# Kernel tuning notes

Measured on AMD Instinct MI355X. Metric: run time of the kernel, lower is better.

Reference implementation:

```python
import jax, jax.numpy as jnp
import numpy as np

BEAM = 8
MAX_LEN = 64
SOS_ID = 1
EOS_ID = 2
NEG = -1e30


def setup_inputs() -> dict:
    key = jax.random.key(0)
    ks = jax.random.split(key, 12)
    B, L, H, V, E = 16, 64, 1024, 32000, 1024
    s = 0.02
    return {
        "dec_hidden": jax.random.normal(ks[0], (B, H), jnp.float32),
        "q_enc_outputs": jax.random.normal(ks[1], (B, L, H), jnp.float32),
        "q_inputs_length": jax.random.randint(ks[2], (B,), 1, L + 1),
        "embedding": jax.random.normal(ks[3], (V, E), jnp.float32) * s,
        "W_ih": jax.random.normal(ks[4], (E, 3 * H), jnp.float32) * s,
        "W_hh": jax.random.normal(ks[5], (H, 3 * H), jnp.float32) * s,
        "b_ih": jnp.zeros((3 * H,), jnp.float32),
        "b_hh": jnp.zeros((3 * H,), jnp.float32),
        "W_c": jax.random.normal(ks[6], (2 * H, H), jnp.float32) * s,
        "W_out": jax.random.normal(ks[7], (H, V), jnp.float32) * s,
        "b_out": jnp.zeros((V,), jnp.float32),
    }


def _beam_search(dec_hidden, q_enc_outputs, q_inputs_length, embedding,
                 W_ih, W_hh, b_ih, b_hh, W_c, W_out, b_out):
    B, H = dec_hidden.shape
    L = q_enc_outputs.shape[1]
    V = W_out.shape[1]
    K = BEAM
    N = B * K
    pos_index = jnp.arange(B)[:, None] * K  # [B,1] offset of each batch's beam block

    # inflate encoder state beam_size times (beam is the inner dim: index = b*K + k)
    hidden = jnp.repeat(dec_hidden, K, axis=0)            # [N,H]
    q_enc = jnp.repeat(q_enc_outputs, K, axis=0)          # [N,L,H]
    q_len = jnp.repeat(q_inputs_length, K, axis=0)        # [N]
    len_mask = jnp.arange(L)[None, :] < q_len[:, None]    # [N,L]

    # only beam 0 of each batch starts live (score 0), rest -inf
    seq_scores = jnp.full((N,), NEG, jnp.float32).at[::K].set(0.0)
    dec_input = jnp.full((N,), SOS_ID, jnp.int32)

    def gru_cell(x, h):
        gx = x @ W_ih + b_ih
        gh = h @ W_hh + b_hh
        xr, xz, xn = jnp.split(gx, 3, axis=-1)
        hr, hz, hn = jnp.split(gh, 3, axis=-1)
        r = jax.nn.sigmoid(xr + hr)
        z = jax.nn.sigmoid(xz + hz)
        n = jnp.tanh(xn + r * hn)
        return (1.0 - z) * n + z * h

    def step(carry, _):
        hidden, seq_scores, dec_input = carry
        x = embedding[dec_input]                               # [N,E]
        h = gru_cell(x, hidden)                                # [N,H]
        # dot-product attention over encoder outputs
        att = jnp.einsum('nh,nlh->nl', h, q_enc) / jnp.sqrt(jnp.float32(H))
        att = jnp.where(len_mask, att, NEG)
        a = jax.nn.softmax(att, axis=-1)
        ctx = jnp.einsum('nl,nlh->nh', a, q_enc)
        o = jnp.tanh(jnp.concatenate([h, ctx], axis=-1) @ W_c)
        logits = o @ W_out + b_out                             # [N,V]
        logp = jax.nn.log_softmax(logits, axis=-1)
        # accumulate scores, flatten beams*vocab per batch, take top-K
        cand = (seq_scores[:, None] + logp).reshape(B, K * V)
        scores, idx = jax.lax.top_k(cand, K)                   # [B,K]
        symbols = (idx % V).reshape(N)
        preds = (idx // V + pos_index).reshape(N)              # predecessor beam rows
        new_hidden = h[preds]
        new_scores = scores.reshape(N)
        stored = new_scores                                     # stored before EOS mask
        new_scores = jnp.where(symbols == EOS_ID, NEG, new_scores)
        return (new_hidden, new_scores, symbols), (stored, preds, symbols)

    _, (all_scores, all_preds, all_syms) = jax.lax.scan(
        step, (hidden, seq_scores, dec_input), None, length=MAX_LEN)

    # backtrack: pick top-K final beams and trace predecessors backwards
    final_scores = all_scores[-1].reshape(B, K)
    sorted_score, sorted_idx = jax.lax.top_k(final_scores, K)
    t_pred = (sorted_idx + pos_index).reshape(N)

    def back(carry, xs):
        syms_t, preds_t = xs
        cur = syms_t[carry]
        return preds_t[carry], cur

    _, seq_rev = jax.lax.scan(back, t_pred, (all_syms[::-1], all_preds[::-1]))
    sequences = seq_rev[::-1].T.reshape(B, BEAM, MAX_LEN)
    return sorted_score, sequences


def reference(dec_hidden, q_enc_outputs, q_inputs_length, embedding,
              W_ih, W_hh, b_ih, b_hh, W_c, W_out, b_out):
    return _beam_search(dec_hidden, q_enc_outputs, q_inputs_length, embedding,
                        W_ih, W_hh, b_ih, b_hh, W_c, W_out, b_out)
```

## Files before the change

### kernel.cpp

```cpp
#include <hip/hip_runtime.h>
#include <cstdint>
#include <cstddef>
#include <climits>

#define Hdim 1024
#define Vdim 32000
#define Lq 64
#define Nrows 128
#define TMAX 64
#define NEGF (-1e30f)

__device__ __forceinline__ bool betterf(float av, int ai, float bv, int bi) {
  return (av > bv) || (av == bv && ai < bi);
}

__device__ __forceinline__ float tanh_xla(float x) {
  float ax = fabsf(x);
  float xc = fminf(fmaxf(x, -7.90531110763549805f), 7.90531110763549805f);
  float x2 = __fmul_rn(xc, xc);
  float p = -2.76076847742355e-16f;
  p = fmaf(p, x2, 2.00018790482477e-13f);
  p = fmaf(p, x2, -8.60467152213735e-11f);
  p = fmaf(p, x2, 5.12229709037114e-08f);
  p = fmaf(p, x2, 1.48572235717979e-05f);
  p = fmaf(p, x2, 6.37261928875436e-04f);
  p = fmaf(p, x2, 4.89352455891786e-03f);
  p = __fmul_rn(xc, p);
  float q = 1.19825839466702e-06f;
  q = fmaf(q, x2, 1.18534705686654e-04f);
  q = fmaf(q, x2, 2.26843463243900e-03f);
  q = fmaf(q, x2, 4.89352518554385e-03f);
  float r = __fdiv_rn(p, q);
  return (ax < 0.0004f) ? x : r;
}

__device__ __forceinline__ float sigmoid_xla(float x) {
  return __fadd_rn(0.5f, __fmul_rn(0.5f, tanh_xla(__fmul_rn(0.5f, x))));
}

__device__ __forceinline__ float exp_xla(float x) {
  x = fminf(x, 88.3762626647950f);
  x = fmaxf(x, -88.3762626647949f);
  float m = floorf(fmaf(x, 1.44269504088896341f, 0.5f));
  float r = fmaf(m, -0.693359375f, x);
  r = fmaf(m, 2.12194440e-4f, r);
  float r2 = __fmul_rn(r, r);
  float p = 1.9875691500e-4f;
  p = fmaf(p, r, 1.3981999507e-3f);
  p = fmaf(p, r, 8.3334519073e-3f);
  p = fmaf(p, r, 4.1665795894e-2f);
  p = fmaf(p, r, 1.6666665459e-1f);
  p = fmaf(p, r, 5.0000001201e-1f);
  p = fmaf(p, r2, r);
  p = __fadd_rn(p, 1.0f);
  int n = (int)m;
  float two_n = __int_as_float((n + 127) << 23);
  return __fmul_rn(p, two_n);
}

__device__ __forceinline__ float log_xla(float x) {
  int ix = __float_as_int(x);
  int e = ((ix >> 23) & 0xFF) - 126;
  float m = __int_as_float((ix & 0x007FFFFF) | 0x3F000000);
  if (m < 0.707106781186547524f) { e -= 1; m = __fadd_rn(m, m); }
  m = __fsub_rn(m, 1.0f);
  float z = __fmul_rn(m, m);
  float p = 7.0376836292e-2f;
  p = fmaf(p, m, -1.1514610310e-1f);
  p = fmaf(p, m, 1.1676998740e-1f);
  p = fmaf(p, m, -1.2420140846e-1f);
  p = fmaf(p, m, 1.4249322787e-1f);
  p = fmaf(p, m, -1.6668057665e-1f);
  p = fmaf(p, m, 2.0000714765e-1f);
  p = fmaf(p, m, -2.4999993993e-1f);
  p = fmaf(p, m, 3.3333331174e-1f);
  float ef = (float)e;
  float y = __fmul_rn(m, __fmul_rn(z, p));
  y = fmaf(ef, -2.12194440e-4f, y);
  y = fmaf(z, -0.5f, y);
  float res = __fadd_rn(m, y);
  res = fmaf(ef, 0.693359375f, res);
  return res;
}

__device__ __forceinline__ int bswz(int col) {
  return col ^ (((col >> 5) & 3) << 2);
}

template <int MT, int NT>
__device__ __forceinline__ void gemm_body(
    const float* __restrict__ A, int lda, const int* __restrict__ rowmap,
    const float* __restrict__ B, int ldb, const float* __restrict__ bias,
    float* __restrict__ C, int ldc, int K, int act, int n0, int m0)
{
  constexpr int RM = MT / 16, RN = NT / 16;
  constexpr int PA = MT + 4, PB = NT + 4;
  __shared__ float As[32][PA];
  __shared__ float Bs[32][PB];
  __shared__ int rows[MT];
  const int t = threadIdx.x;
  if (t < MT) rows[t] = rowmap ? rowmap[m0 + t] : (m0 + t);
  __syncthreads();
  const int tm = t >> 4, tn = t & 15;
  float acc[RM][RN] = {};
  for (int kt = 0; kt < K; kt += 32) {
#pragma unroll
    for (int i = 0; i < MT / 32; ++i) {
      int idx = t + i * 256;
      int m = idx >> 3, k4 = idx & 7;
      float4 v = *reinterpret_cast<const float4*>(
          &A[(size_t)rows[m] * lda + (size_t)(kt + k4 * 4)]);
      As[k4 * 4 + 0][m] = v.x;
      As[k4 * 4 + 1][m] = v.y;
      As[k4 * 4 + 2][m] = v.z;
      As[k4 * 4 + 3][m] = v.w;
    }
#pragma unroll
    for (int i = 0; i < NT / 32; ++i) {
      int idx = t + i * 256;
      int kk = idx / (NT / 4), n4 = idx % (NT / 4);
      float4 v = *reinterpret_cast<const float4*>(
          &B[(size_t)(kt + kk) * ldb + (size_t)(n0 + n4 * 4)]);
      *reinterpret_cast<float4*>(&Bs[kk][bswz(n4 * 4)]) = v;
    }
    __syncthreads();
#pragma unroll
    for (int kk = 0; kk < 32; ++kk) {
      float a[RM], bb[RN];
      if constexpr (RM == 2) {
        float2 v = *reinterpret_cast<const float2*>(&As[kk][tm * 2]);
        a[0] = v.x; a[1] = v.y;
      } else {
#pragma unroll
        for (int c = 0; c < RM / 4; ++c) {
          float4 v = *reinterpret_cast<const float4*>(&As[kk][tm * RM + c * 4]);
          a[c * 4 + 0] = v.x; a[c * 4 + 1] = v.y;
          a[c * 4 + 2] = v.z; a[c * 4 + 3] = v.w;
        }
      }
      if constexpr (RN == 2) {
        float2 v = *reinterpret_cast<const float2*>(&Bs[kk][tn * 2]);
        bb[0] = v.x; bb[1] = v.y;
      } else {
#pragma unroll
        for (int c = 0; c < RN / 4; ++c) {
          float4 v = *reinterpret_cast<const float4*>(
              &Bs[kk][bswz(tn * RN + c * 4)]);
          bb[c * 4 + 0] = v.x; bb[c * 4 + 1] = v.y;
          bb[c * 4 + 2] = v.z; bb[c * 4 + 3] = v.w;
        }
      }
#pragma unroll
      for (int i = 0; i < RM; ++i)
#pragma unroll
        for (int j = 0; j < RN; ++j)
          acc[i][j] = fmaf(a[i], bb[j], acc[i][j]);
    }
    __syncthreads();
  }
#pragma unroll
  for (int i = 0; i < RM; ++i) {
    int m = m0 + tm * RM + i;
#pragma unroll
    for (int j = 0; j < RN; ++j) {
      int n = n0 + tn * RN + j;
      float v = acc[i][j];
      if (bias) v = __fadd_rn(v, bias[n]);
      if (act == 1) v = tanh_xla(v);
      C[(size_t)m * ldc + n] = v;
    }
  }
}

__global__ __launch_bounds__(128, 2) void sgemm_logits(
    const float* __restrict__ A, const float* __restrict__ B,
    const float* __restrict__ bias, float* __restrict__ C)
{
  constexpr int MT = 128, NT = 128, RM = 8, RN = 16;
  constexpr int PA = MT + 4, PB = NT + 4;
  __shared__ float As[32][PA];
  __shared__ float Bs[32][PB];
  const int t = threadIdx.x;
  const int n0 = blockIdx.x * NT;
  const int tm = t >> 3, tn = t & 7;
  float acc[RM][RN] = {};
  for (int kt = 0; kt < 1024; kt += 32) {
#pragma unroll
    for (int i = 0; i < 8; ++i) {
      int idx = t + i * 128;
      int m = idx >> 3, k4 = idx & 7;
      float4 v = *reinterpret_cast<const float4*>(
          &A[(size_t)m * 1024 + (size_t)(kt + k4 * 4)]);
      As[k4 * 4 + 0][m] = v.x;
      As[k4 * 4 + 1][m] = v.y;
      As[k4 * 4 + 2][m] = v.z;
      As[k4 * 4 + 3][m] = v.w;
    }
#pragma unroll
    for (int i = 0; i < 8; ++i) {
      int idx = t + i * 128;
      int kk = idx >> 5, n4 = idx & 31;
      float4 v = *reinterpret_cast<const float4*>(
          &B[(size_t)(kt + kk) * 32000 + (size_t)(n0 + n4 * 4)]);
      *reinterpret_cast<float4*>(&Bs[kk][bswz(n4 * 4)]) = v;
    }
    __syncthreads();
#pragma unroll
    for (int kk = 0; kk < 32; ++kk) {
      float a[RM], bb[RN];
#pragma unroll
      for (int c = 0; c < 2; ++c) {
        float4 v = *reinterpret_cast<const float4*>(&As[kk][tm * RM + c * 4]);
        a[c * 4 + 0] = v.x; a[c * 4 + 1] = v.y;
        a[c * 4 + 2] = v.z; a[c * 4 + 3] = v.w;
      }
#pragma unroll
      for (int c = 0; c < 4; ++c) {
        float4 v = *reinterpret_cast<const float4*>(
            &Bs[kk][bswz(tn * RN + c * 4)]);
        bb[c * 4 + 0] = v.x; bb[c * 4 + 1] = v.y;
        bb[c * 4 + 2] = v.z; bb[c * 4 + 3] = v.w;
      }
#pragma unroll
      for (int i = 0; i < RM; ++i)
#pragma unroll
        for (int j = 0; j < RN; ++j)
          acc[i][j] = fmaf(a[i], bb[j], acc[i][j]);
    }
    __syncthreads();
  }
#pragma unroll
  for (int i = 0; i < RM; ++i) {
    int m = tm * RM + i;
#pragma unroll
    for (int j = 0; j < RN; ++j) {
      int n = n0 + tn * RN + j;
      float v = __fadd_rn(acc[i][j], bias[n]);
      C[(size_t)m * 32000 + n] = v;
    }
  }
}

__global__ __launch_bounds__(256) void gates_gemm(
    const float* __restrict__ emb, const int* __restrict__ symmap,
    const float* __restrict__ W_ih,
    const float* __restrict__ hprev, const int* __restrict__ hmap,
    const float* __restrict__ W_hh,
    float* __restrict__ gA, float* __restrict__ gB)
{
  if (blockIdx.z == 0)
    gemm_body<32, 64>(emb, 1024, symmap, W_ih, 3072, nullptr, gA, 3072, 1024, 0,
                      blockIdx.x * 64, blockIdx.y * 32);
  else
    gemm_body<32, 64>(hprev, 1024, hmap, W_hh, 3072, nullptr, gB, 3072, 1024, 0,
                      blockIdx.x * 64, blockIdx.y * 32);
}

__global__ __launch_bounds__(256) void sgemm_wc(
    const float* __restrict__ A2, const float* __restrict__ W_c,
    float* __restrict__ obuf)
{
  gemm_body<32, 32>(A2, 2048, nullptr, W_c, 1024, nullptr, obuf, 1024, 2048, 1,
                    blockIdx.x * 32, blockIdx.y * 32);
}

__global__ __launch_bounds__(256) void gru_attn(
    const float* __restrict__ gA, const float* __restrict__ gB,
    const float* __restrict__ b_ih, const float* __restrict__ b_hh,
    const float* __restrict__ hprev, const int* __restrict__ hmap,
    const float* __restrict__ q_enc, const int* __restrict__ q_len,
    float* __restrict__ hout, float* __restrict__ A2)
{
  int n = blockIdx.x;
  int b = n >> 3;
  int t = threadIdx.x;
  __shared__ float hsh[Hdim];
  __shared__ float att[Lq];
  __shared__ float ebuf[Lq];
  __shared__ float s_mx, s_sum;

  {
    int row = hmap[n];
    const float* hp = hprev + (size_t)row * Hdim;
    const float* a = gA + (size_t)n * 3 * Hdim;
    const float* g = gB + (size_t)n * 3 * Hdim;
    for (int j = t; j < Hdim; j += 256) {
      float xr = __fadd_rn(a[j],            b_ih[j]);
      float xz = __fadd_rn(a[Hdim + j],     b_ih[Hdim + j]);
      float xn = __fadd_rn(a[2 * Hdim + j], b_ih[2 * Hdim + j]);
      float hr = __fadd_rn(g[j],            b_hh[j]);
      float hz = __fadd_rn(g[Hdim + j],     b_hh[Hdim + j]);
      float hn = __fadd_rn(g[2 * Hdim + j], b_hh[2 * Hdim + j]);
      float r = sigmoid_xla(__fadd_rn(xr, hr));
      float z = sigmoid_xla(__fadd_rn(xz, hz));
      float t1 = __fmul_rn(r, hn);
      float nn = tanh_xla(__fadd_rn(xn, t1));
      float u1 = __fsub_rn(1.0f, z);
      float u2 = __fmul_rn(u1, nn);
      float u3 = __fmul_rn(z, hp[j]);
      float h = __fadd_rn(u2, u3);
      hout[(size_t)n * Hdim + j] = h;
      A2[(size_t)n * 2 * Hdim + j] = h;
      hsh[j] = h;
    }
  }
  __syncthreads();

  const float* q = q_enc + (size_t)b * Lq * Hdim;
  if (t < Lq) {
    const float4* h4 = reinterpret_cast<const float4*>(hsh);
    const float4* q4 = reinterpret_cast<const float4*>(q + (size_t)t * Hdim);
    float acc[8];
#pragma unroll
    for (int j = 0; j < 8; ++j) acc[j] = 0.f;
    for (int i = 0; i < 128; ++i) {
      float4 ha = h4[2 * i], hb = h4[2 * i + 1];
      float4 qa = q4[2 * i], qb = q4[2 * i + 1];
      acc[0] = fmaf(ha.x, qa.x, acc[0]);
      acc[1] = fmaf(ha.y, qa.y, acc[1]);
      acc[2] = fmaf(ha.z, qa.z, acc[2]);
      acc[3] = fmaf(ha.w, qa.w, acc[3]);
      acc[4] = fmaf(hb.x, qb.x, acc[4]);
      acc[5] = fmaf(hb.y, qb.y, acc[5]);
      acc[6] = fmaf(hb.z, qb.z, acc[6]);
      acc[7] = fmaf(hb.w, qb.w, acc[7]);
    }
    float b0 = __fadd_rn(acc[0], acc[4]);
    float b1 = __fadd_rn(acc[1], acc[5]);
    float b2 = __fadd_rn(acc[2], acc[6]);
    float b3 = __fadd_rn(acc[3], acc[7]);
    float c0 = __fadd_rn(b0, b2);
    float c1 = __fadd_rn(b1, b3);
    float dot = __fadd_rn(c0, c1);
    att[t] = __fdiv_rn(dot, 32.0f);
  }
  __syncthreads();
  if (t == 0) {
    int len = q_len[b];
    float mx = -INFINITY;
    for (int l = 0; l < Lq; ++l) {
      float v = (l < len) ? att[l] : NEGF;
      att[l] = v;
      mx = fmaxf(mx, v);
    }
    s_mx = mx;
  }
  __syncthreads();
  if (t < Lq) ebuf[t] = exp_xla(__fsub_rn(att[t], s_mx));
  __syncthreads();
  if (t == 0) {
    float acc[8];
#pragma unroll
    for (int j = 0; j < 8; ++j) acc[j] = 0.f;
    for (int i = 0; i < 8; ++i) {
#pragma unroll
      for (int j = 0; j < 8; ++j) acc[j] = __fadd_rn(acc[j], ebuf[i * 8 + j]);
    }
    float b0 = __fadd_rn(acc[0], acc[4]);
    float b1 = __fadd_rn(acc[1], acc[5]);
    float b2 = __fadd_rn(acc[2], acc[6]);
    float b3 = __fadd_rn(acc[3], acc[7]);
    float c0 = __fadd_rn(b0, b2);
    float c1 = __fadd_rn(b1, b3);
    s_sum = __fadd_rn(c0, c1);
  }
  __syncthreads();
  if (t < Lq) att[t] = __fdiv_rn(ebuf[t], s_sum);
  __syncthreads();
#pragma unroll
  for (int hh = 0; hh < 4; ++hh) {
    int h = t + hh * 256;
    float c = 0.f;
    for (int l = 0; l < Lq; ++l) c = fmaf(att[l], q[(size_t)l * Hdim + h], c);
    A2[(size_t)n * 2 * Hdim + Hdim + h] = c;
  }
}

__global__ __launch_bounds__(256) void lse_kernel(const float* __restrict__ logits,
                                                  float* __restrict__ ebuf,
                                                  float* __restrict__ mxA,
                                                  float* __restrict__ lseA)
{
  int n = blockIdx.x;
  const float* row = logits + (size_t)n * Vdim;
  float* erow = ebuf + (size_t)n * Vdim;
  int t = threadIdx.x;
  int lane = t & 63, w = t >> 6;
  const float4* row4 = reinterpret_cast<const float4*>(row);
  float4* erow4 = reinterpret_cast<float4*>(erow);
  float mx = -INFINITY;
  for (int i = t; i < 8000; i += 256) {
    float4 v = row4[i];
    mx = fmaxf(mx, fmaxf(fmaxf(v.x, v.y), fmaxf(v.z, v.w)));
  }
#pragma unroll
  for (int off = 32; off >= 1; off >>= 1) mx = fmaxf(mx, __shfl_xor(mx, off, 64));
  __shared__ float sm[4];
  __shared__ float lanes[8];
  if (lane == 0) sm[w] = mx;
  __syncthreads();
  mx = fmaxf(fmaxf(sm[0], sm[1]), fmaxf(sm[2], sm[3]));
  for (int i = t; i < 8000; i += 256) {
    float4 v = row4[i];
    float4 e;
    e.x = exp_xla(__fsub_rn(v.x, mx));
    e.y = exp_xla(__fsub_rn(v.y, mx));
    e.z = exp_xla(__fsub_rn(v.z, mx));
    e.w = exp_xla(__fsub_rn(v.w, mx));
    erow4[i] = e;
  }
  __syncthreads();
  if (t < 8) {
    float a = 0.f;
#pragma unroll 8
    for (int i = 0; i < 4000; ++i) a = __fadd_rn(a, erow[i * 8 + t]);
    lanes[t] = a;
  }
  __syncthreads();
  if (t == 0) {
    float b0 = __fadd_rn(lanes[0], lanes[4]);
    float b1 = __fadd_rn(lanes[1], lanes[5]);
    float b2 = __fadd_rn(lanes[2], lanes[6]);
    float b3 = __fadd_rn(lanes[3], lanes[7]);
    float c0 = __fadd_rn(b0, b2);
    float c1 = __fadd_rn(b1, b3);
    float s = __fadd_rn(c0, c1);
    mxA[n] = mx;
    lseA[n] = log_xla(s);
  }
}

__global__ __launch_bounds__(256) void topk_kernel(
    const float* __restrict__ logits, const float* __restrict__ mxA,
    const float* __restrict__ lseA, float* __restrict__ seq_scores,
    float* __restrict__ all_scores, int* __restrict__ all_preds,
    int* __restrict__ all_syms, int step)
{
  int b = blockIdx.x, t = threadIdx.x;
  __shared__ float s_seq[8], s_mx[8], s_lse[8];
  if (t < 8) {
    s_seq[t] = seq_scores[b * 8 + t];
    s_mx[t] = mxA[b * 8 + t];
    s_lse[t] = lseA[b * 8 + t];
  }
  __syncthreads();
  float lv[8]; int li[8];
#pragma unroll
  for (int r = 0; r < 8; ++r) { lv[r] = -INFINITY; li[r] = INT_MAX; }
  const float4* base4 = reinterpret_cast<const float4*>(logits + (size_t)b * 8 * Vdim);
  for (int c4 = t; c4 < 64000; c4 += 256) {
    float4 v4 = base4[c4];
    int cb = c4 * 4;
#pragma unroll
    for (int e = 0; e < 4; ++e) {
      int c = cb + e;
      int k = c / Vdim;
      float x = (e == 0) ? v4.x : (e == 1) ? v4.y : (e == 2) ? v4.z : v4.w;
      float sh = __fsub_rn(x, s_mx[k]);
      float lp = __fsub_rn(sh, s_lse[k]);
      float cand = __fadd_rn(s_seq[k], lp);
      if (betterf(cand, c, lv[7], li[7])) {
        lv[7] = cand; li[7] = c;
#pragma unroll
        for (int r = 7; r > 0; --r) {
          if (betterf(lv[r], li[r], lv[r - 1], li[r - 1])) {
            float tv = lv[r]; lv[r] = lv[r - 1]; lv[r - 1] = tv;
            int ti = li[r]; li[r] = li[r - 1]; li[r - 1] = ti;
          }
        }
      }
    }
  }
  __shared__ float sv[256][8];
  __shared__ int si[256][8];
#pragma unroll
  for (int r = 0; r < 8; ++r) { sv[t][r] = lv[r]; si[t][r] = li[r]; }
  __syncthreads();
  if (t == 0) {
    for (int u = 1; u < 256; ++u) {
#pragma unroll
      for (int r = 0; r < 8; ++r) {
        float v = sv[u][r]; int ix = si[u][r];
        if (betterf(v, ix, lv[7], li[7])) {
          lv[7] = v; li[7] = ix;
#pragma unroll
          for (int q = 7; q > 0; --q) {
            if (betterf(lv[q], li[q], lv[q - 1], li[q - 1])) {
              float tv = lv[q]; lv[q] = lv[q - 1]; lv[q - 1] = tv;
              int ti = li[q]; li[q] = li[q - 1]; li[q - 1] = ti;
            }
          }
        } else break;
      }
    }
#pragma unroll
    for (int r = 0; r < 8; ++r) {
      int idx = li[r];
      int sym = idx % Vdim;
      int pred = idx / Vdim + b * 8;
      int n = b * 8 + r;
      all_scores[step * Nrows + n] = lv[r];
      all_preds[step * Nrows + n] = pred;
      all_syms[step * Nrows + n] = sym;
      seq_scores[n] = (sym == 2) ? NEGF : lv[r];
    }
  }
}

__global__ void init_kernel(float* seq_scores, int* init_hmap, int* init_sym) {
  int t = threadIdx.x;
  if (t < 128) {
    seq_scores[t] = ((t & 7) == 0) ? 0.0f : NEGF;
    init_hmap[t] = t >> 3;
    init_sym[t] = 1;
  }
}

__global__ void final_topk(const float* __restrict__ all_scores,
                           int* __restrict__ tpred, float* __restrict__ out_scores) {
  int b = threadIdx.x;
  if (b >= 16) return;
  float v[8]; int ki[8];
#pragma unroll
  for (int k = 0; k < 8; ++k) { v[k] = all_scores[63 * Nrows + b * 8 + k]; ki[k] = k; }
#pragma unroll
  for (int p = 0; p < 7; ++p)
#pragma unroll
    for (int i = 0; i < 7; ++i) {
      if (!betterf(v[i], ki[i], v[i + 1], ki[i + 1])) {
        float tv = v[i]; v[i] = v[i + 1]; v[i + 1] = tv;
        int ti = ki[i]; ki[i] = ki[i + 1]; ki[i + 1] = ti;
      }
    }
#pragma unroll
  for (int j = 0; j < 8; ++j) {
    out_scores[b * 8 + j] = v[j];
    tpred[b * 8 + j] = b * 8 + ki[j];
  }
}

__global__ void backtrack(const int* __restrict__ all_syms, const int* __restrict__ all_preds,
                          const int* __restrict__ tpred, float* __restrict__ out_seq) {
  int n = threadIdx.x;
  if (n >= 128) return;
  int carry = tpred[n];
  for (int tt = 63; tt >= 0; --tt) {
    int sym = all_syms[tt * Nrows + carry];
    out_seq[(size_t)n * 64 + tt] = (float)sym;
    carry = all_preds[tt * Nrows + carry];
  }
}

extern "C" void kernel_launch(void* const* d_in, const int* in_sizes, int n_in,
                              void* d_out, int out_size, void* d_ws, size_t ws_size,
                              hipStream_t stream) {
  (void)in_sizes; (void)n_in; (void)out_size; (void)ws_size;
  const float* dec_hidden = (const float*)d_in[0];
  const float* q_enc      = (const float*)d_in[1];
  const int*   q_len      = (const int*)d_in[2];
  const float* embedding  = (const float*)d_in[3];
  const float* W_ih       = (const float*)d_in[4];
  const float* W_hh       = (const float*)d_in[5];
  const float* b_ih       = (const float*)d_in[6];
  const float* b_hh       = (const float*)d_in[7];
  const float* W_c        = (const float*)d_in[8];
  const float* W_out      = (const float*)d_in[9];
  const float* b_out      = (const float*)d_in[10];
  float* out_scores = (float*)d_out;
  float* out_seq    = (float*)d_out + 128;

  char* w = (char*)d_ws;
  auto alloc = [&](size_t bytes) {
    char* p = w;
    w += (bytes + 255) & ~(size_t)255;
    return p;
  };
  float* hbuf0 = (float*)alloc((size_t)128 * 1024 * 4);
  float* hbuf1 = (float*)alloc((size_t)128 * 1024 * 4);
  float* A2    = (float*)alloc((size_t)128 * 2048 * 4);
  float* obuf  = (float*)alloc((size_t)128 * 1024 * 4);
  float* gA    = (float*)alloc((size_t)128 * 3072 * 4);
  float* gB    = (float*)alloc((size_t)128 * 3072 * 4);
  float* logits = (float*)alloc((size_t)128 * 32000 * 4);
  float* ebuf   = (float*)alloc((size_t)128 * 32000 * 4);
  float* mxA   = (float*)alloc(128 * 4);
  float* lseA  = (float*)alloc(128 * 4);
  float* seq_scores = (float*)alloc(128 * 4);
  int* init_hmap = (int*)alloc(128 * 4);
  int* init_sym  = (int*)alloc(128 * 4);
  int* tpred     = (int*)alloc(128 * 4);
  float* all_scores = (float*)alloc((size_t)64 * 128 * 4);
  int* all_preds = (int*)alloc((size_t)64 * 128 * 4);
  int* all_syms  = (int*)alloc((size_t)64 * 128 * 4);

  init_kernel<<<1, 128, 0, stream>>>(seq_scores, init_hmap, init_sym);

  for (int t = 0; t < TMAX; ++t) {
    const int* symmap = (t == 0) ? init_sym : (all_syms + (t - 1) * Nrows);
    const int* hmap   = (t == 0) ? init_hmap : (all_preds + (t - 1) * Nrows);
    const float* hprev = (t == 0) ? dec_hidden : (((t - 1) & 1) ? hbuf1 : hbuf0);
    float* hcur = (t & 1) ? hbuf1 : hbuf0;

    gates_gemm<<<dim3(48, 4, 2), 256, 0, stream>>>(
        embedding, symmap, W_ih, hprev, hmap, W_hh, gA, gB);
    gru_attn<<<128, 256, 0, stream>>>(gA, gB, b_ih, b_hh, hprev, hmap,
                                      q_enc, q_len, hcur, A2);
    sgemm_wc<<<dim3(32, 4), 256, 0, stream>>>(A2, W_c, obuf);
    sgemm_logits<<<250, 128, 0, stream>>>(obuf, W_out, b_out, logits);
    lse_kernel<<<128, 256, 0, stream>>>(logits, ebuf, mxA, lseA);
    topk_kernel<<<16, 256, 0, stream>>>(logits, mxA, lseA, seq_scores,
                                        all_scores, all_preds, all_syms, t);
  }

  final_topk<<<1, 128, 0, stream>>>(all_scores, tpred, out_scores);
  backtrack<<<1, 128, 0, stream>>>(all_syms, all_preds, tpred, out_seq);
}
```

Measured before the change: 67.31 ms.

## Double-buffer logits GEMM loads via registers and use 256 threads per block

```diff
diff --git a/kernel.cpp b/kernel.cpp
--- a/kernel.cpp
+++ b/kernel.cpp
@@ -172,39 +172,58 @@
   }
 }
 
-__global__ __launch_bounds__(128, 2) void sgemm_logits(
+__global__ __launch_bounds__(256) void sgemm_logits(
     const float* __restrict__ A, const float* __restrict__ B,
     const float* __restrict__ bias, float* __restrict__ C)
 {
-  constexpr int MT = 128, NT = 128, RM = 8, RN = 16;
-  constexpr int PA = MT + 4, PB = NT + 4;
-  __shared__ float As[32][PA];
-  __shared__ float Bs[32][PB];
+  constexpr int RM = 8, RN = 8;
+  __shared__ float As[32][132];
+  __shared__ float Bs[32][132];
   const int t = threadIdx.x;
-  const int n0 = blockIdx.x * NT;
-  const int tm = t >> 3, tn = t & 7;
+  const int n0 = blockIdx.x * 128;
+  const int tm = t >> 4, tn = t & 15;
+  float4 rA[4], rB[4];
+
+  auto load_regs = [&](int kt) {
+#pragma unroll
+    for (int i = 0; i < 4; ++i) {
+      int idx = t + i * 256;
+      int m = idx >> 3, k4 = idx & 7;
+      rA[i] = *reinterpret_cast<const float4*>(
+          &A[(size_t)m * 1024 + (size_t)(kt + k4 * 4)]);
+    }
+#pragma unroll
+    for (int i = 0; i < 4; ++i) {
+      int idx = t + i * 256;
+      int kk = idx >> 5, n4 = idx & 31;
+      rB[i] = *reinterpret_cast<const float4*>(
+          &B[(size_t)(kt + kk) * 32000 + (size_t)(n0 + n4 * 4)]);
+    }
+  };
+  auto store_lds = [&]() {
+#pragma unroll
+    for (int i = 0; i < 4; ++i) {
+      int idx = t + i * 256;
+      int m = idx >> 3, k4 = idx & 7;
+      As[k4 * 4 + 0][m] = rA[i].x;
+      As[k4 * 4 + 1][m] = rA[i].y;
+      As[k4 * 4 + 2][m] = rA[i].z;
+      As[k4 * 4 + 3][m] = rA[i].w;
+    }
+#pragma unroll
+    for (int i = 0; i < 4; ++i) {
+      int idx = t + i * 256;
+      int kk = idx >> 5, n4 = idx & 31;
+      *reinterpret_cast<float4*>(&Bs[kk][bswz(n4 * 4)]) = rB[i];
+    }
+  };
+
   float acc[RM][RN] = {};
-  for (int kt = 0; kt < 1024; kt += 32) {
-#pragma unroll
-    for (int i = 0; i < 8; ++i) {
-      int idx = t + i * 128;
-      int m = idx >> 3, k4 = idx & 7;
-      float4 v = *reinterpret_cast<const float4*>(
-          &A[(size_t)m * 1024 + (size_t)(kt + k4 * 4)]);
-      As[k4 * 4 + 0][m] = v.x;
-      As[k4 * 4 + 1][m] = v.y;
-      As[k4 * 4 + 2][m] = v.z;
-      As[k4 * 4 + 3][m] = v.w;
-    }
-#pragma unroll
-    for (int i = 0; i < 8; ++i) {
-      int idx = t + i * 128;
-      int kk = idx >> 5, n4 = idx & 31;
-      float4 v = *reinterpret_cast<const float4*>(
-          &B[(size_t)(kt + kk) * 32000 + (size_t)(n0 + n4 * 4)]);
-      *reinterpret_cast<float4*>(&Bs[kk][bswz(n4 * 4)]) = v;
-    }
-    __syncthreads();
+  load_regs(0);
+  store_lds();
+  __syncthreads();
+  for (int tile = 0; tile < 32; ++tile) {
+    if (tile < 31) load_regs((tile + 1) * 32);
 #pragma unroll
     for (int kk = 0; kk < 32; ++kk) {
       float a[RM], bb[RN];
@@ -215,7 +234,7 @@
         a[c * 4 + 2] = v.z; a[c * 4 + 3] = v.w;
       }
 #pragma unroll
-      for (int c = 0; c < 4; ++c) {
+      for (int c = 0; c < 2; ++c) {
         float4 v = *reinterpret_cast<const float4*>(
             &Bs[kk][bswz(tn * RN + c * 4)]);
         bb[c * 4 + 0] = v.x; bb[c * 4 + 1] = v.y;
@@ -227,6 +246,8 @@
         for (int j = 0; j < RN; ++j)
           acc[i][j] = fmaf(a[i], bb[j], acc[i][j]);
     }
+    __syncthreads();
+    if (tile < 31) store_lds();
     __syncthreads();
   }
 #pragma unroll
@@ -606,7 +627,7 @@
     gru_attn<<<128, 256, 0, stream>>>(gA, gB, b_ih, b_hh, hprev, hmap,
                                       q_enc, q_len, hcur, A2);
     sgemm_wc<<<dim3(32, 4), 256, 0, stream>>>(A2, W_c, obuf);
-    sgemm_logits<<<250, 128, 0, stream>>>(obuf, W_out, b_out, logits);
+    sgemm_logits<<<250, 256, 0, stream>>>(obuf, W_out, b_out, logits);
     lse_kernel<<<128, 256, 0, stream>>>(logits, ebuf, mxA, lseA);
     topk_kernel<<<16, 256, 0, stream>>>(logits, mxA, lseA, seq_scores,
                                         all_scores, all_preds, all_syms, t);
```

New measurement: 92.38 ms. 37.2% more time.
